# Kernel tuning notes

Measured on AMD Instinct MI355X. Metric: run time of the kernel, lower is better.

The kernel has to match this reference:

```python
import jax, jax.numpy as jnp
import numpy as np

E, H, DK, DV = 768, 12, 64, 64
S, B = 8, 1024


def setup_inputs() -> dict:
    key = jax.random.key(0)
    ks = jax.random.split(key, 12)
    std = 1.0 / np.sqrt(E)
    inp = {
        "Q": jax.random.normal(ks[0], (S, B, E), jnp.float32),
        "K": jax.random.normal(ks[1], (S, B, E), jnp.float32),
        "V": jax.random.normal(ks[2], (S, B, E), jnp.float32),
        # projection weights, torch Linear convention: y = x @ W.T + b
        "Wq": jax.random.normal(ks[3], (H * DK, E), jnp.float32) * std,
        "bq": jax.random.normal(ks[4], (H * DK,), jnp.float32) * std,
        "Wk": jax.random.normal(ks[5], (H * DK, E), jnp.float32) * std,
        "bk": jax.random.normal(ks[6], (H * DK,), jnp.float32) * std,
        "Wv": jax.random.normal(ks[7], (H * DV, E), jnp.float32) * std,
        "bv": jax.random.normal(ks[8], (H * DV,), jnp.float32) * std,
        "Wo": jax.random.normal(ks[9], (E, H * DV), jnp.float32) * std,
        "bo": jax.random.normal(ks[10], (E,), jnp.float32) * std,
        "ln_g": jnp.ones((E,), jnp.float32),
        "ln_b": jnp.zeros((E,), jnp.float32),
    }
    return inp


def _attention(Q, K, V, Wq, bq, Wk, bk, Wv, bv, Wo, bo, ln_g, ln_b):
    s, b, _ = Q.shape
    # linear projections, then view(S,B,H,d).transpose(1,2) -> [S,H,B,d]
    q = (Q @ Wq.T + bq).reshape(s, b, H, DK).transpose(0, 2, 1, 3)
    k = (K @ Wk.T + bk).reshape(s, b, H, DK).transpose(0, 2, 1, 3)
    v = (V @ Wv.T + bv).reshape(s, b, H, DV).transpose(0, 2, 1, 3)
    # scores over the batch (size-B) axis: [S,H,B,B]
    scores = jnp.einsum("shbd,shcd->shbc", q, k) / jnp.sqrt(
        jnp.asarray(DK, jnp.float32))
    attn = jax.nn.softmax(scores, axis=-1)
    context = jnp.einsum("shbc,shcd->shbd", attn, v)  # [S,H,B,DV]
    context = context.transpose(0, 2, 1, 3).reshape(s, b, H * DV)
    out = context @ Wo.T + bo
    x = out + Q  # residual
    mu = jnp.mean(x, axis=-1, keepdims=True)
    var = jnp.mean((x - mu) ** 2, axis=-1, keepdims=True)
    normed = (x - mu) * jax.lax.rsqrt(var + 1e-5) * ln_g + ln_b
    return normed, attn


def reference(Q, K, V, Wq, bq, Wk, bk, Wv, bv, Wo, bo, ln_g, ln_b):
    return _attention(Q, K, V, Wq, bq, Wk, bk, Wv, bv, Wo, bo, ln_g, ln_b)
```

## Files before the change

kernel.cpp:

```cpp
#include <hip/hip_runtime.h>
#include <hip/hip_bf16.h>
#include <math.h>

#define Sd 8
#define Bd 1024
#define Ed 768
#define Hd 12
#define Dd 64
#define SBd 8192

typedef short bf16x8 __attribute__((ext_vector_type(8)));
typedef unsigned short u16x8 __attribute__((ext_vector_type(8)));
typedef float f32x4 __attribute__((ext_vector_type(4)));

#define QSC 0.18033688011112043f

#define BARRIER()                                        \
  do {                                                   \
    asm volatile("s_waitcnt lgkmcnt(0)" ::: "memory");   \
    __builtin_amdgcn_s_barrier();                        \
    asm volatile("" ::: "memory");                       \
  } while (0)

static __device__ __forceinline__ unsigned short f2bf(float f) {
  unsigned int u = __builtin_bit_cast(unsigned int, f);
  u += 0x7fffu + ((u >> 16) & 1u);
  return (unsigned short)(u >> 16);
}

static __device__ __forceinline__ unsigned int pk2(float lo, float hi) {
  return (unsigned int)f2bf(lo) | ((unsigned int)f2bf(hi) << 16);
}

__global__ __launch_bounds__(256, 2) void qkv_kernel(
    const float* __restrict__ Qin, const float* __restrict__ Kin,
    const float* __restrict__ Vin,
    const float* __restrict__ Wq, const float* __restrict__ bq,
    const float* __restrict__ Wk, const float* __restrict__ bk,
    const float* __restrict__ Wv, const float* __restrict__ bv,
    unsigned short* __restrict__ qo, unsigned short* __restrict__ ko,
    unsigned short* __restrict__ vo) {
  __shared__ unsigned short As[128 * 72];
  __shared__ unsigned short Bs[128 * 72];
  const float* X;
  const float* W;
  const float* bias;
  switch (blockIdx.z) {
    case 0: X = Qin; W = Wq; bias = bq; break;
    case 1: X = Kin; W = Wk; bias = bk; break;
    default: X = Vin; W = Wv; bias = bv; break;
  }
  const int i0 = blockIdx.x * 128;
  const int j0 = blockIdx.y * 128;
  const int t = threadIdx.x;
  const int w = t >> 6, l = t & 63, lr = l & 15, lg = l >> 4;
  const int wr = w >> 1, wc = w & 1;

  f32x4 acc[4][4] = {};

  for (int k0 = 0; k0 < Ed; k0 += 64) {
    uint2 pa[8], pb[8];
#pragma unroll
    for (int q = 0; q < 8; ++q) {
      int flat = t + 256 * q;
      int row = flat >> 4;
      int c4 = (flat & 15) * 4;
      float4 va = *(const float4*)(X + (size_t)(i0 + row) * Ed + k0 + c4);
      float4 vb = *(const float4*)(W + (size_t)(j0 + row) * Ed + k0 + c4);
      pa[q] = make_uint2(pk2(va.x, va.y), pk2(va.z, va.w));
      pb[q] = make_uint2(pk2(vb.x, vb.y), pk2(vb.z, vb.w));
    }
    __syncthreads();
#pragma unroll
    for (int q = 0; q < 8; ++q) {
      int flat = t + 256 * q;
      int row = flat >> 4;
      int c4 = (flat & 15) * 4;
      *(uint2*)&As[row * 72 + c4] = pa[q];
      *(uint2*)&Bs[row * 72 + c4] = pb[q];
    }
    __syncthreads();
#pragma unroll
    for (int ks = 0; ks < 2; ++ks) {
      bf16x8 af[4], bf[4];
#pragma unroll
      for (int fr = 0; fr < 4; ++fr)
        af[fr] = *(const bf16x8*)&As[(wr * 64 + fr * 16 + lr) * 72 + ks * 32 + lg * 8];
#pragma unroll
      for (int fc = 0; fc < 4; ++fc)
        bf[fc] = *(const bf16x8*)&Bs[(wc * 64 + fc * 16 + lr) * 72 + ks * 32 + lg * 8];
#pragma unroll
      for (int fr = 0; fr < 4; ++fr)
#pragma unroll
        for (int fc = 0; fc < 4; ++fc)
          acc[fr][fc] = __builtin_amdgcn_mfma_f32_16x16x32_bf16(af[fr], bf[fc], acc[fr][fc], 0, 0, 0);
    }
  }

  const int z = blockIdx.z;
  if (z < 2) {
    unsigned short* out = (z == 0) ? qo : ko;
    const float sc = (z == 0) ? QSC : 1.0f;
#pragma unroll
    for (int fr = 0; fr < 4; ++fr) {
#pragma unroll
      for (int fc = 0; fc < 4; ++fc) {
        int colg = j0 + wc * 64 + fc * 16 + lr;
        int h = colg >> 6, d = colg & 63;
        float bv_ = bias[colg];
#pragma unroll
        for (int r = 0; r < 4; ++r) {
          int i = i0 + wr * 64 + fr * 16 + lg * 4 + r;
          int s = i >> 10, b = i & 1023;
          float v = (acc[fr][fc][r] + bv_) * sc;
          out[((((size_t)s * Hd + h) * Bd + b) << 6) + d] = f2bf(v);
        }
      }
    }
  } else {
#pragma unroll
    for (int fr = 0; fr < 4; ++fr) {
#pragma unroll
      for (int fc = 0; fc < 4; ++fc) {
        int colg = j0 + wc * 64 + fc * 16 + lr;
        int h = colg >> 6, d = colg & 63;
        float bv_ = bias[colg];
#pragma unroll
        for (int r = 0; r < 4; ++r) {
          int i = i0 + wr * 64 + fr * 16 + lg * 4 + r;
          int s = i >> 10, b = i & 1023;
          float v = acc[fr][fc][r] + bv_;
          vo[(((size_t)s * Hd + h) * 64 + d) * Bd + b] = f2bf(v);
        }
      }
    }
  }
}

__global__ __launch_bounds__(256) void attn_kernel(
    const unsigned short* __restrict__ qb, const unsigned short* __restrict__ kb,
    const unsigned short* __restrict__ vt, float* __restrict__ attn_out,
    unsigned short* __restrict__ ctx_out) {
  __shared__ unsigned short Ks[64 * 72];
  __shared__ unsigned short Vs[64 * 72];
  __shared__ unsigned short Pb[4][16 * 72];
  const int sh = blockIdx.y;
  const int s = sh / Hd, h = sh % Hd;
  const int row0 = blockIdx.x * 64;
  const size_t base = (size_t)sh * Bd * 64;
  const int t = threadIdx.x;
  const int w = t >> 6, l = t & 63, lr = l & 15, lg = l >> 4;
  const int srow = t >> 2, skg = (t & 3) << 4;

  const int qrow = row0 + w * 16 + lr;
  const bf16x8 aq0 = *(const bf16x8*)(qb + base + (size_t)qrow * 64 + lg * 8);
  const bf16x8 aq1 = *(const bf16x8*)(qb + base + (size_t)qrow * 64 + 32 + lg * 8);

  float lsum[4] = {0.f, 0.f, 0.f, 0.f};

  {
    const unsigned short* kp = kb + base + (size_t)srow * 64 + skg;
    u16x8 k0 = *(const u16x8*)kp;
    u16x8 k1 = *(const u16x8*)(kp + 8);
    for (int ct = 0; ct < 16; ++ct) {
      BARRIER();
      *(u16x8*)&Ks[srow * 72 + skg] = k0;
      *(u16x8*)&Ks[srow * 72 + skg + 8] = k1;
      BARRIER();
      if (ct < 15) {
        const unsigned short* kn = kb + base + (size_t)((ct + 1) * 64 + srow) * 64 + skg;
        k0 = *(const u16x8*)kn;
        k1 = *(const u16x8*)(kn + 8);
      }
      f32x4 scv[4] = {};
#pragma unroll
      for (int ks = 0; ks < 2; ++ks) {
        bf16x8 a = ks ? aq1 : aq0;
#pragma unroll
        for (int c2 = 0; c2 < 4; ++c2) {
          bf16x8 bb = *(const bf16x8*)&Ks[(c2 * 16 + lr) * 72 + ks * 32 + lg * 8];
          scv[c2] = __builtin_amdgcn_mfma_f32_16x16x32_bf16(a, bb, scv[c2], 0, 0, 0);
        }
      }
#pragma unroll
      for (int c2 = 0; c2 < 4; ++c2)
#pragma unroll
        for (int r = 0; r < 4; ++r)
          lsum[r] += __builtin_amdgcn_exp2f(scv[c2][r]);
    }
  }
#pragma unroll
  for (int r = 0; r < 4; ++r) {
    float s1 = lsum[r];
    s1 += __shfl_xor(s1, 1, 16);
    s1 += __shfl_xor(s1, 2, 16);
    s1 += __shfl_xor(s1, 4, 16);
    s1 += __shfl_xor(s1, 8, 16);
    lsum[r] = 1.0f / s1;
  }

  f32x4 cacc[4] = {};
  const unsigned short* vbase = vt + (size_t)sh * 64 * Bd;
  u16x8 k0, k1, v0, v1;
  {
    const unsigned short* kp = kb + base + (size_t)srow * 64 + skg;
    k0 = *(const u16x8*)kp;
    k1 = *(const u16x8*)(kp + 8);
    const unsigned short* vp = vbase + (size_t)srow * Bd + skg;
    v0 = *(const u16x8*)vp;
    v1 = *(const u16x8*)(vp + 8);
  }
  for (int ct = 0; ct < 16; ++ct) {
    BARRIER();
    *(u16x8*)&Ks[srow * 72 + skg] = k0;
    *(u16x8*)&Ks[srow * 72 + skg + 8] = k1;
    *(u16x8*)&Vs[srow * 72 + skg] = v0;
    *(u16x8*)&Vs[srow * 72 + skg + 8] = v1;
    BARRIER();
    if (ct < 15) {
      const unsigned short* kn = kb + base + (size_t)((ct + 1) * 64 + srow) * 64 + skg;
      k0 = *(const u16x8*)kn;
      k1 = *(const u16x8*)(kn + 8);
      const unsigned short* vn = vbase + (size_t)srow * Bd + (ct + 1) * 64 + skg;
      v0 = *(const u16x8*)vn;
      v1 = *(const u16x8*)(vn + 8);
    }
    f32x4 scv[4] = {};
#pragma unroll
    for (int ks = 0; ks < 2; ++ks) {
      bf16x8 a = ks ? aq1 : aq0;
#pragma unroll
      for (int c2 = 0; c2 < 4; ++c2) {
        bf16x8 bb = *(const bf16x8*)&Ks[(c2 * 16 + lr) * 72 + ks * 32 + lg * 8];
        scv[c2] = __builtin_amdgcn_mfma_f32_16x16x32_bf16(a, bb, scv[c2], 0, 0, 0);
      }
    }
#pragma unroll
    for (int c2 = 0; c2 < 4; ++c2) {
#pragma unroll
      for (int r = 0; r < 4; ++r) {
        float p = __builtin_amdgcn_exp2f(scv[c2][r]) * lsum[r];
        int row = row0 + w * 16 + lg * 4 + r;
        __builtin_nontemporal_store(
            p, &attn_out[((size_t)sh * Bd + row) * Bd + ct * 64 + c2 * 16 + lr]);
        Pb[w][(lg * 4 + r) * 72 + c2 * 16 + lr] = f2bf(p);
      }
    }
#pragma unroll
    for (int ks2 = 0; ks2 < 2; ++ks2) {
      bf16x8 pa = *(const bf16x8*)&Pb[w][lr * 72 + ks2 * 32 + lg * 8];
#pragma unroll
      for (int dt = 0; dt < 4; ++dt) {
        bf16x8 bv = *(const bf16x8*)&Vs[(dt * 16 + lr) * 72 + ks2 * 32 + lg * 8];
        cacc[dt] = __builtin_amdgcn_mfma_f32_16x16x32_bf16(pa, bv, cacc[dt], 0, 0, 0);
      }
    }
  }

#pragma unroll
  for (int dt = 0; dt < 4; ++dt) {
#pragma unroll
    for (int r = 0; r < 4; ++r) {
      int row = row0 + w * 16 + lg * 4 + r;
      size_t i = (size_t)s * Bd + row;
      int j = h * 64 + dt * 16 + lr;
      ctx_out[i * Ed + j] = f2bf(cacc[dt][r]);
    }
  }
}

__global__ __launch_bounds__(256, 2) void proj_kernel(
    const unsigned short* __restrict__ ctx, const float* __restrict__ Wo,
    const float* __restrict__ bo, const float* __restrict__ Qin,
    float* __restrict__ xout) {
  __shared__ unsigned short As[128 * 72];
  __shared__ unsigned short Bs[128 * 72];
  const int i0 = blockIdx.x * 128;
  const int j0 = blockIdx.y * 128;
  const int t = threadIdx.x;
  const int w = t >> 6, l = t & 63, lr = l & 15, lg = l >> 4;
  const int wr = w >> 1, wc = w & 1;

  f32x4 acc[4][4] = {};

  for (int k0 = 0; k0 < Ed; k0 += 64) {
    u16x8 pa[4];
    uint2 pb[8];
#pragma unroll
    for (int q = 0; q < 4; ++q) {
      int flat = t + 256 * q;
      int row = flat >> 3;
      int c8 = (flat & 7) * 8;
      pa[q] = *(const u16x8*)(ctx + (size_t)(i0 + row) * Ed + k0 + c8);
    }
#pragma unroll
    for (int q = 0; q < 8; ++q) {
      int flat = t + 256 * q;
      int row = flat >> 4;
      int c4 = (flat & 15) * 4;
      float4 vb = *(const float4*)(Wo + (size_t)(j0 + row) * Ed + k0 + c4);
      pb[q] = make_uint2(pk2(vb.x, vb.y), pk2(vb.z, vb.w));
    }
    __syncthreads();
#pragma unroll
    for (int q = 0; q < 4; ++q) {
      int flat = t + 256 * q;
      int row = flat >> 3;
      int c8 = (flat & 7) * 8;
      *(u16x8*)&As[row * 72 + c8] = pa[q];
    }
#pragma unroll
    for (int q = 0; q < 8; ++q) {
      int flat = t + 256 * q;
      int row = flat >> 4;
      int c4 = (flat & 15) * 4;
      *(uint2*)&Bs[row * 72 + c4] = pb[q];
    }
    __syncthreads();
#pragma unroll
    for (int ks = 0; ks < 2; ++ks) {
      bf16x8 af[4], bf[4];
#pragma unroll
      for (int fr = 0; fr < 4; ++fr)
        af[fr] = *(const bf16x8*)&As[(wr * 64 + fr * 16 + lr) * 72 + ks * 32 + lg * 8];
#pragma unroll
      for (int fc = 0; fc < 4; ++fc)
        bf[fc] = *(const bf16x8*)&Bs[(wc * 64 + fc * 16 + lr) * 72 + ks * 32 + lg * 8];
#pragma unroll
      for (int fr = 0; fr < 4; ++fr)
#pragma unroll
        for (int fc = 0; fc < 4; ++fc)
          acc[fr][fc] = __builtin_amdgcn_mfma_f32_16x16x32_bf16(af[fr], bf[fc], acc[fr][fc], 0, 0, 0);
    }
  }

#pragma unroll
  for (int fr = 0; fr < 4; ++fr) {
#pragma unroll
    for (int fc = 0; fc < 4; ++fc) {
      int j = j0 + wc * 64 + fc * 16 + lr;
      float bv_ = bo[j];
#pragma unroll
      for (int r = 0; r < 4; ++r) {
        int i = i0 + wr * 64 + fr * 16 + lg * 4 + r;
        float v = acc[fr][fc][r] + bv_ + Qin[(size_t)i * Ed + j];
        xout[(size_t)i * Ed + j] = v;
      }
    }
  }
}

__global__ __launch_bounds__(256) void ln_kernel(
    const float* __restrict__ x, const float* __restrict__ g,
    const float* __restrict__ bb, float* __restrict__ out) {
  const int i = blockIdx.x;
  const int t = threadIdx.x;
  const float* xr = x + (size_t)i * Ed;
  float v0 = xr[t], v1 = xr[t + 256], v2 = xr[t + 512];
  float s1 = v0 + v1 + v2;
  float s2 = v0 * v0 + v1 * v1 + v2 * v2;
#pragma unroll
  for (int mk = 1; mk < 64; mk <<= 1) {
    s1 += __shfl_xor(s1, mk, 64);
    s2 += __shfl_xor(s2, mk, 64);
  }
  __shared__ float red[8];
  const int w = t >> 6, l = t & 63;
  if (l == 0) { red[w] = s1; red[w + 4] = s2; }
  __syncthreads();
  s1 = red[0] + red[1] + red[2] + red[3];
  s2 = red[4] + red[5] + red[6] + red[7];
  float mu = s1 * (1.0f / 768.0f);
  float var = s2 * (1.0f / 768.0f) - mu * mu;
  float rs = rsqrtf(var + 1e-5f);
  float* orow = out + (size_t)i * Ed;
  orow[t] = (v0 - mu) * rs * g[t] + bb[t];
  orow[t + 256] = (v1 - mu) * rs * g[t + 256] + bb[t + 256];
  orow[t + 512] = (v2 - mu) * rs * g[t + 512] + bb[t + 512];
}

extern "C" void kernel_launch(void* const* d_in, const int* in_sizes, int n_in,
                              void* d_out, int out_size, void* d_ws, size_t ws_size,
                              hipStream_t stream) {
  (void)in_sizes; (void)n_in; (void)out_size; (void)ws_size;
  const float* Qin = (const float*)d_in[0];
  const float* Kin = (const float*)d_in[1];
  const float* Vin = (const float*)d_in[2];
  const float* Wq = (const float*)d_in[3];
  const float* bq = (const float*)d_in[4];
  const float* Wk = (const float*)d_in[5];
  const float* bk = (const float*)d_in[6];
  const float* Wv = (const float*)d_in[7];
  const float* bv = (const float*)d_in[8];
  const float* Wo = (const float*)d_in[9];
  const float* bo = (const float*)d_in[10];
  const float* ln_g = (const float*)d_in[11];
  const float* ln_b = (const float*)d_in[12];

  float* outp = (float*)d_out;
  float* normed = outp;
  float* attn_out = outp + (size_t)SBd * Ed;

  char* ws = (char*)d_ws;
  unsigned short* qws = (unsigned short*)ws;
  unsigned short* kws = qws + 6291456;
  unsigned short* vws = kws + 6291456;
  unsigned short* ctxws = vws + 6291456;
  float* xws = (float*)(ws + (size_t)4 * 12582912);

  dim3 blk(256);
  hipLaunchKernelGGL(qkv_kernel, dim3(64, 6, 3), blk, 0, stream,
                     Qin, Kin, Vin, Wq, bq, Wk, bk, Wv, bv, qws, kws, vws);
  hipLaunchKernelGGL(attn_kernel, dim3(16, 96), blk, 0, stream,
                     qws, kws, vws, attn_out, ctxws);
  hipLaunchKernelGGL(proj_kernel, dim3(64, 6), blk, 0, stream,
                     ctxws, Wo, bo, Qin, xws);
  hipLaunchKernelGGL(ln_kernel, dim3(8192), blk, 0, stream,
                     xws, ln_g, ln_b, normed);
}
```

Measured before the change: 290.5 us.

## Fuse softmax into single pass with deferred normalization of stored probabilities

Drops the separate first pass over K that only computed softmax row sums. The kernel now runs one pass: it accumulates row sums while doing P·V on unnormalized exponentials, and keeps the probabilities packed as bf16 in registers. At the end it normalizes both the context and the attention-matrix writes. This halves the QK^T MFMA work and the K traffic, but adds about 128 VGPRs of register storage, which risks spills or lower occupancy. It also rounds the stored attention probabilities to bf16 before scaling, and pushes all attention writes to the kernel tail.

```diff
diff --git a/kernel.cpp b/kernel.cpp
--- a/kernel.cpp
+++ b/kernel.cpp
@@ -30,6 +30,13 @@
 
 static __device__ __forceinline__ unsigned int pk2(float lo, float hi) {
   return (unsigned int)f2bf(lo) | ((unsigned int)f2bf(hi) << 16);
+}
+
+static __device__ __forceinline__ float bflo(unsigned int u) {
+  return __builtin_bit_cast(float, u << 16);
+}
+static __device__ __forceinline__ float bfhi(unsigned int u) {
+  return __builtin_bit_cast(float, u & 0xffff0000u);
 }
 
 __global__ __launch_bounds__(256, 2) void qkv_kernel(
@@ -157,50 +164,10 @@
   const bf16x8 aq1 = *(const bf16x8*)(qb + base + (size_t)qrow * 64 + 32 + lg * 8);
 
   float lsum[4] = {0.f, 0.f, 0.f, 0.f};
-
-  {
-    const unsigned short* kp = kb + base + (size_t)srow * 64 + skg;
-    u16x8 k0 = *(const u16x8*)kp;
-    u16x8 k1 = *(const u16x8*)(kp + 8);
-    for (int ct = 0; ct < 16; ++ct) {
-      BARRIER();
-      *(u16x8*)&Ks[srow * 72 + skg] = k0;
-      *(u16x8*)&Ks[srow * 72 + skg + 8] = k1;
-      BARRIER();
-      if (ct < 15) {
-        const unsigned short* kn = kb + base + (size_t)((ct + 1) * 64 + srow) * 64 + skg;
-        k0 = *(const u16x8*)kn;
-        k1 = *(const u16x8*)(kn + 8);
-      }
-      f32x4 scv[4] = {};
-#pragma unroll
-      for (int ks = 0; ks < 2; ++ks) {
-        bf16x8 a = ks ? aq1 : aq0;
-#pragma unroll
-        for (int c2 = 0; c2 < 4; ++c2) {
-          bf16x8 bb = *(const bf16x8*)&Ks[(c2 * 16 + lr) * 72 + ks * 32 + lg * 8];
-          scv[c2] = __builtin_amdgcn_mfma_f32_16x16x32_bf16(a, bb, scv[c2], 0, 0, 0);
-        }
-      }
-#pragma unroll
-      for (int c2 = 0; c2 < 4; ++c2)
-#pragma unroll
-        for (int r = 0; r < 4; ++r)
-          lsum[r] += __builtin_amdgcn_exp2f(scv[c2][r]);
-    }
-  }
-#pragma unroll
-  for (int r = 0; r < 4; ++r) {
-    float s1 = lsum[r];
-    s1 += __shfl_xor(s1, 1, 16);
-    s1 += __shfl_xor(s1, 2, 16);
-    s1 += __shfl_xor(s1, 4, 16);
-    s1 += __shfl_xor(s1, 8, 16);
-    lsum[r] = 1.0f / s1;
-  }
-
+  uint2 pst[16][4];
   f32x4 cacc[4] = {};
   const unsigned short* vbase = vt + (size_t)sh * 64 * Bd;
+
   u16x8 k0, k1, v0, v1;
   {
     const unsigned short* kp = kb + base + (size_t)srow * 64 + skg;
@@ -210,6 +177,7 @@
     v0 = *(const u16x8*)vp;
     v1 = *(const u16x8*)(vp + 8);
   }
+#pragma unroll
   for (int ct = 0; ct < 16; ++ct) {
     BARRIER();
     *(u16x8*)&Ks[srow * 72 + skg] = k0;
@@ -237,14 +205,17 @@
     }
 #pragma unroll
     for (int c2 = 0; c2 < 4; ++c2) {
-#pragma unroll
-      for (int r = 0; r < 4; ++r) {
-        float p = __builtin_amdgcn_exp2f(scv[c2][r]) * lsum[r];
-        int row = row0 + w * 16 + lg * 4 + r;
-        __builtin_nontemporal_store(
-            p, &attn_out[((size_t)sh * Bd + row) * Bd + ct * 64 + c2 * 16 + lr]);
-        Pb[w][(lg * 4 + r) * 72 + c2 * 16 + lr] = f2bf(p);
-      }
+      float p0 = __builtin_amdgcn_exp2f(scv[c2][0]);
+      float p1 = __builtin_amdgcn_exp2f(scv[c2][1]);
+      float p2 = __builtin_amdgcn_exp2f(scv[c2][2]);
+      float p3 = __builtin_amdgcn_exp2f(scv[c2][3]);
+      lsum[0] += p0; lsum[1] += p1; lsum[2] += p2; lsum[3] += p3;
+      uint2 pp = make_uint2(pk2(p0, p1), pk2(p2, p3));
+      pst[ct][c2] = pp;
+      Pb[w][(lg * 4 + 0) * 72 + c2 * 16 + lr] = (unsigned short)(pp.x & 0xffffu);
+      Pb[w][(lg * 4 + 1) * 72 + c2 * 16 + lr] = (unsigned short)(pp.x >> 16);
+      Pb[w][(lg * 4 + 2) * 72 + c2 * 16 + lr] = (unsigned short)(pp.y & 0xffffu);
+      Pb[w][(lg * 4 + 3) * 72 + c2 * 16 + lr] = (unsigned short)(pp.y >> 16);
     }
 #pragma unroll
     for (int ks2 = 0; ks2 < 2; ++ks2) {
@@ -257,6 +228,17 @@
     }
   }
 
+  float invl[4];
+#pragma unroll
+  for (int r = 0; r < 4; ++r) {
+    float s1 = lsum[r];
+    s1 += __shfl_xor(s1, 1, 16);
+    s1 += __shfl_xor(s1, 2, 16);
+    s1 += __shfl_xor(s1, 4, 16);
+    s1 += __shfl_xor(s1, 8, 16);
+    invl[r] = 1.0f / s1;
+  }
+
 #pragma unroll
   for (int dt = 0; dt < 4; ++dt) {
 #pragma unroll
@@ -264,7 +246,21 @@
       int row = row0 + w * 16 + lg * 4 + r;
       size_t i = (size_t)s * Bd + row;
       int j = h * 64 + dt * 16 + lr;
-      ctx_out[i * Ed + j] = f2bf(cacc[dt][r]);
+      ctx_out[i * Ed + j] = f2bf(cacc[dt][r] * invl[r]);
+    }
+  }
+
+  float* arow = attn_out + ((size_t)sh * Bd + row0 + w * 16 + lg * 4) * Bd + lr;
+#pragma unroll
+  for (int ct = 0; ct < 16; ++ct) {
+#pragma unroll
+    for (int c2 = 0; c2 < 4; ++c2) {
+      uint2 pp = pst[ct][c2];
+      int cb = ct * 64 + c2 * 16;
+      __builtin_nontemporal_store(bflo(pp.x) * invl[0], arow + (size_t)0 * Bd + cb);
+      __builtin_nontemporal_store(bfhi(pp.x) * invl[1], arow + (size_t)1 * Bd + cb);
+      __builtin_nontemporal_store(bflo(pp.y) * invl[2], arow + (size_t)2 * Bd + cb);
+      __builtin_nontemporal_store(bfhi(pp.y) * invl[3], arow + (size_t)3 * Bd + cb);
     }
   }
 }
```

Result: slower. 347.5 us (+19.6%).
